# Kernel optimization log

Measured on AMD Instinct MI355X. Metric: run time of the kernel, lower is better.

The kernel has to match this reference:

```python
import jax, jax.numpy as jnp
import numpy as np

N = 131072          # batch of latents
IN_DIM = 64         # in_dim
EMB = 64            # embedding_size
K = 1024            # num_embeddings (codebook size)
DENSE = 2 * (IN_DIM + EMB)  # 256, hidden width of encoder/decoder MLPs


def _linear_params(key, fan_in, fan_out):
    # equinox Linear default init: uniform(-1/sqrt(fan_in), 1/sqrt(fan_in))
    kw, kb = jax.random.split(key)
    lim = 1.0 / np.sqrt(fan_in)
    W = jax.random.uniform(kw, (fan_out, fan_in), minval=-lim, maxval=lim, dtype=jnp.float32)
    b = jax.random.uniform(kb, (fan_out,), minval=-lim, maxval=lim, dtype=jnp.float32)
    return W, b


def setup_inputs() -> dict:
    key = jax.random.key(0)
    ks = jax.random.split(key, 8)
    x = jax.random.normal(ks[0], (N, IN_DIM), dtype=jnp.float32)
    We1, be1 = _linear_params(ks[1], IN_DIM, DENSE)
    We2, be2 = _linear_params(ks[2], DENSE, DENSE)
    We3, be3 = _linear_params(ks[3], DENSE, EMB)
    Wd1, bd1 = _linear_params(ks[4], EMB, DENSE)
    Wd2, bd2 = _linear_params(ks[5], DENSE, DENSE)
    Wd3, bd3 = _linear_params(ks[6], DENSE, IN_DIM)
    emb = jax.random.normal(ks[7], (K, EMB), dtype=jnp.float32) / 1000.0
    return dict(x=x, We1=We1, be1=be1, We2=We2, be2=be2, We3=We3, be3=be3,
                emb=emb, Wd1=Wd1, bd1=bd1, Wd2=Wd2, bd2=bd2, Wd3=Wd3, bd3=bd3)


def reference(x, We1, be1, We2, be2, We3, be3, emb, Wd1, bd1, Wd2, bd2, Wd3, bd3):
    selu = jax.nn.selu
    # encoder: Linear -> selu -> Linear -> selu -> Linear   (batched via matmul)
    h = selu(x @ We1.T + be1)
    h = selu(h @ We2.T + be2)
    z = h @ We3.T + be3                      # [N, EMB]
    # quantize: squared distance to every codebook row, argmin, straight-through
    # ||z - e||^2 expanded to avoid materializing [N, K, EMB]
    d = (jnp.sum(z * z, axis=1, keepdims=True)
         - 2.0 * (z @ emb.T)
         + jnp.sum(emb * emb, axis=1))       # [N, K]
    idx = jnp.argmin(d, axis=1)              # [N] int
    zq = z + jax.lax.stop_gradient(emb[idx] - z)   # straight-through lookup
    # decoder
    h = selu(zq @ Wd1.T + bd1)
    h = selu(h @ Wd2.T + bd2)
    recon = h @ Wd3.T + bd3                  # [N, IN_DIM]
    return recon, idx
```

## Files before the change

### kernel.cpp

```cpp
#include <hip/hip_runtime.h>
#include <math.h>

#pragma clang fp contract(off)

#define NROWS 131072

__device__ __forceinline__ float selu_f(float v) {
    float em  = expm1f(v);
    float neg = 1.6732632423543772f * em;
    float r   = v > 0.0f ? v : neg;
    return 1.0507009873554805f * r;
}

__device__ __forceinline__ float4 ldf4(const float* p) { return *(const float4*)p; }

__device__ __forceinline__ void ld4x4(float4* b, const float* p) {
    b[0] = ldf4(p); b[1] = ldf4(p + 4); b[2] = ldf4(p + 8); b[3] = ldf4(p + 12);
}

__device__ __forceinline__ void fma16a(float* a, const float4* w, float h) {
    a[0]  = __builtin_fmaf(w[0].x, h, a[0]);  a[1]  = __builtin_fmaf(w[0].y, h, a[1]);
    a[2]  = __builtin_fmaf(w[0].z, h, a[2]);  a[3]  = __builtin_fmaf(w[0].w, h, a[3]);
    a[4]  = __builtin_fmaf(w[1].x, h, a[4]);  a[5]  = __builtin_fmaf(w[1].y, h, a[5]);
    a[6]  = __builtin_fmaf(w[1].z, h, a[6]);  a[7]  = __builtin_fmaf(w[1].w, h, a[7]);
    a[8]  = __builtin_fmaf(w[2].x, h, a[8]);  a[9]  = __builtin_fmaf(w[2].y, h, a[9]);
    a[10] = __builtin_fmaf(w[2].z, h, a[10]); a[11] = __builtin_fmaf(w[2].w, h, a[11]);
    a[12] = __builtin_fmaf(w[3].x, h, a[12]); a[13] = __builtin_fmaf(w[3].y, h, a[13]);
    a[14] = __builtin_fmaf(w[3].z, h, a[14]); a[15] = __builtin_fmaf(w[3].w, h, a[15]);
}

__device__ __forceinline__ void step16(float* acc, float4* wb, const float* nextp, float h) {
    float4 t0 = ldf4(nextp), t1 = ldf4(nextp + 4), t2 = ldf4(nextp + 8), t3 = ldf4(nextp + 12);
    fma16a(acc, wb, h);
    wb[0] = t0; wb[1] = t1; wb[2] = t2; wb[3] = t3;
}

__device__ __forceinline__ void fma16q(float* a, float4 w0, float4 w1, float4 w2, float4 w3, float h) {
    a[0]  = __builtin_fmaf(w0.x, h, a[0]);  a[1]  = __builtin_fmaf(w0.y, h, a[1]);
    a[2]  = __builtin_fmaf(w0.z, h, a[2]);  a[3]  = __builtin_fmaf(w0.w, h, a[3]);
    a[4]  = __builtin_fmaf(w1.x, h, a[4]);  a[5]  = __builtin_fmaf(w1.y, h, a[5]);
    a[6]  = __builtin_fmaf(w1.z, h, a[6]);  a[7]  = __builtin_fmaf(w1.w, h, a[7]);
    a[8]  = __builtin_fmaf(w2.x, h, a[8]);  a[9]  = __builtin_fmaf(w2.y, h, a[9]);
    a[10] = __builtin_fmaf(w2.z, h, a[10]); a[11] = __builtin_fmaf(w2.w, h, a[11]);
    a[12] = __builtin_fmaf(w3.x, h, a[12]); a[13] = __builtin_fmaf(w3.y, h, a[13]);
    a[14] = __builtin_fmaf(w3.z, h, a[14]); a[15] = __builtin_fmaf(w3.w, h, a[15]);
}

typedef __attribute__((address_space(3))) unsigned int lds_u32;
typedef const __attribute__((address_space(1))) unsigned int glb_u32;
__device__ __forceinline__ void gll16(const float* g, float* l) {
    __builtin_amdgcn_global_load_lds((glb_u32*)g, (lds_u32*)l, 16, 0, 0);
}

__global__ void prep_transpose(const float* __restrict__ W1, const float* __restrict__ W2,
                               const float* __restrict__ W3,
                               float* __restrict__ W1T, float* __restrict__ W2T,
                               float* __restrict__ W3T) {
    int id = blockIdx.x * 256 + threadIdx.x;
    if (id < 65536) { int c = id >> 8, j = id & 255; W2T[j * 256 + c] = W2[id]; }
    int id2 = id - 65536;
    if (id2 >= 0 && id2 < 16384) { int e = id2 >> 8, c = id2 & 255; W3T[c * 64 + e] = W3[id2]; }
    int id3 = id - 81920;
    if (id3 >= 0 && id3 < 16384) { int c = id3 >> 6, j = id3 & 63; W1T[j * 256 + c] = W1[id3]; }
}

__global__ void prep_decoder(const float* __restrict__ emb,
                             const float* __restrict__ Wd1, const float* __restrict__ bd1,
                             const float* __restrict__ Wd2, const float* __restrict__ bd2,
                             const float* __restrict__ Wd3, const float* __restrict__ bd3,
                             float* __restrict__ dec_out, float* __restrict__ en) {
    __shared__ float e[64];
    __shared__ float h1[256];
    __shared__ float h2[256];
    const int t = threadIdx.x;
    for (int kc = 0; kc < 4; ++kc) {
        const int k = blockIdx.x * 4 + kc;
        __syncthreads();
        if (t < 64) e[t] = emb[k * 64 + t];
        __syncthreads();
        {
            float acc = 0.0f;
            const float* w = Wd1 + t * 64;
            #pragma unroll
            for (int j = 0; j < 64; ++j) acc = __builtin_fmaf(w[j], e[j], acc);
            h1[t] = selu_f(acc + bd1[t]);
        }
        __syncthreads();
        {
            float acc = 0.0f;
            const float* w = Wd2 + t * 256;
            #pragma unroll 8
            for (int j = 0; j < 256; ++j) acc = __builtin_fmaf(w[j], h1[j], acc);
            h2[t] = selu_f(acc + bd2[t]);
        }
        __syncthreads();
        if (t < 64) {
            float acc = 0.0f;
            const float* w = Wd3 + t * 256;
            #pragma unroll 8
            for (int j = 0; j < 256; ++j) acc = __builtin_fmaf(w[j], h2[j], acc);
            dec_out[k * 64 + t] = acc + bd3[t];
        }
        if (t == 0) {
            float r[8];
            #pragma unroll
            for (int u = 0; u < 8; ++u) r[u] = e[u] * e[u];
            #pragma unroll
            for (int i = 8; i < 64; i += 8) {
                #pragma unroll
                for (int u = 0; u < 8; ++u) { float p = e[i + u] * e[i + u]; r[u] = r[u] + p; }
            }
            en[k] = ((r[0] + r[1]) + (r[2] + r[3])) + ((r[4] + r[5]) + (r[6] + r[7]));
        }
    }
}

__global__ __launch_bounds__(256) __attribute__((amdgpu_waves_per_eu(2, 8)))
void vqvae_main(const float* __restrict__ x,
                const float* __restrict__ b1, const float* __restrict__ b2,
                const float* __restrict__ b3,
                const float* __restrict__ W1T, const float* __restrict__ W2T,
                const float* __restrict__ W3T,
                const float* __restrict__ emb, const float* __restrict__ en,
                const float* __restrict__ dec_out, float* __restrict__ out) {
    __shared__ __align__(16) float B0[4096];
    __shared__ __align__(16) float B1[4352];
    __shared__ __align__(16) float B2[4096];

    const int t    = threadIdx.x;
    const int wave = t >> 6;
    const int lane = t & 63;
    const size_t rowbase = (size_t)blockIdx.x * 64;

    int lz;
    asm volatile("v_mov_b32 %0, 0" : "=v"(lz));

    const float* W1Tv = W1T + lz;
    const float* W2Tv = W2T + lz;
    const float* W3Tv = W3T + lz;
    const float* b1v  = b1 + lz;
    const float* b2v  = b2 + lz;
    const float* b3v  = b3 + lz;
    const float* env  = en + lz;
    const float* embv = emb + lz;

    #pragma unroll
    for (int q = 0; q < 4; ++q) {
        int f = t + 256 * q;
        int r = f >> 4, c4 = f & 15;
        float4 v = ldf4(x + (rowbase + r) * 64 + c4 * 4);
        B0[(c4 * 4 + 0) * 64 + r] = v.x;
        B0[(c4 * 4 + 1) * 64 + r] = v.y;
        B0[(c4 * 4 + 2) * 64 + r] = v.z;
        B0[(c4 * 4 + 3) * 64 + r] = v.w;
    }
    __syncthreads();

    float acc2[64];
    #pragma unroll
    for (int u = 0; u < 64; ++u) acc2[u] = 0.0f;

    for (int cc = 0; cc < 4; ++cc) {
        {
            const float* wp = W1Tv + cc * 64 + wave * 16;
            float4 A[4];
            ld4x4(A, wp);
            float acc[16];
            #pragma unroll
            for (int u = 0; u < 16; ++u) acc[u] = 0.0f;
            #pragma unroll 1
            for (int j = 0; j < 64; ++j) {
                const float* np = wp + (j + 1) * 256;
                step16(acc, A, np, B0[j * 64 + lane]);
            }
            float bb[16];
            *(float4*)&bb[0]  = ldf4(b1v + cc * 64 + wave * 16);
            *(float4*)&bb[4]  = ldf4(b1v + cc * 64 + wave * 16 + 4);
            *(float4*)&bb[8]  = ldf4(b1v + cc * 64 + wave * 16 + 8);
            *(float4*)&bb[12] = ldf4(b1v + cc * 64 + wave * 16 + 12);
            float hv[16];
            #pragma unroll
            for (int u = 0; u < 16; ++u) hv[u] = selu_f(acc[u] + bb[u]);
            #pragma unroll
            for (int up = 0; up < 8; ++up) {
                *(float2*)&B1[(wave * 8 + up) * 128 + (lane << 1)] =
                    make_float2(hv[2 * up], hv[2 * up + 1]);
            }
        }
        __syncthreads();
        {
            const float* gsrc = W2Tv + (size_t)(cc * 64 + (lane >> 4)) * 256 + wave * 64 + (lane & 15) * 4;
            float* stA = B2 + wave * 1024;
            gll16(gsrc, stA);
            gll16(gsrc + 1024, stA + 256);
            #pragma unroll 1
            for (int s = 0; s < 8; ++s) {
                if (s < 7) {
                    const float* ns = gsrc + (size_t)(s + 1) * 2048;
                    float* nd = stA + ((s + 1) & 1) * 512;
                    gll16(ns, nd);
                    gll16(ns + 1024, nd + 256);
                    asm volatile("s_waitcnt vmcnt(2)" ::: "memory");
                } else {
                    asm volatile("s_waitcnt vmcnt(0)" ::: "memory");
                }
                const float* wl = stA + (s & 1) * 512;
                #pragma unroll
                for (int jj = 0; jj < 8; jj += 2) {
                    float2 h01 = *(const float2*)&B1[((s * 8 + jj) >> 1) * 128 + (lane << 1)];
                    const float* r0 = wl + jj * 64;
                    #pragma unroll
                    for (int qd = 0; qd < 4; ++qd) {
                        const float* p = r0 + qd * 16;
                        fma16q(acc2 + qd * 16, ldf4(p), ldf4(p + 4), ldf4(p + 8), ldf4(p + 12), h01.x);
                    }
                    const float* r1 = wl + (jj + 1) * 64;
                    #pragma unroll
                    for (int qd = 0; qd < 4; ++qd) {
                        const float* p = r1 + qd * 16;
                        fma16q(acc2 + qd * 16, ldf4(p), ldf4(p + 4), ldf4(p + 8), ldf4(p + 12), h01.y);
                    }
                }
            }
        }
        __syncthreads();
    }

    {
        #pragma unroll
        for (int qd = 0; qd < 4; ++qd) {
            float bb[16];
            *(float4*)&bb[0]  = ldf4(b2v + wave * 64 + qd * 16);
            *(float4*)&bb[4]  = ldf4(b2v + wave * 64 + qd * 16 + 4);
            *(float4*)&bb[8]  = ldf4(b2v + wave * 64 + qd * 16 + 8);
            *(float4*)&bb[12] = ldf4(b2v + wave * 64 + qd * 16 + 12);
            #pragma unroll
            for (int i = 0; i < 16; ++i)
                acc2[qd * 16 + i] = selu_f(acc2[qd * 16 + i] + bb[i]);
        }
    }

    const int er = wave * 16;
    float s01[16], s23[16];
    for (int g = 0; g < 4; ++g) {
        if (wave == g) {
            #pragma unroll
            for (int u = 0; u < 64; ++u) B0[u * 64 + lane] = acc2[u];
        }
        __syncthreads();
        const float* w3p = W3Tv + g * 4096 + er;
        float4 F0[4], F1[4];
        ld4x4(F0, w3p); ld4x4(F1, w3p + 64);
        float P[16];
        #pragma unroll
        for (int u = 0; u < 16; ++u) P[u] = 0.0f;
        #pragma unroll 1
        for (int c = 0; c < 64; c += 2) {
            const float* np = w3p + (c + 2) * 64;
            step16(P, F0, np,      B0[(c + 0) * 64 + lane]);
            step16(P, F1, np + 64, B0[(c + 1) * 64 + lane]);
        }
        if (g == 0) {
            #pragma unroll
            for (int u = 0; u < 16; ++u) s01[u] = P[u];
        } else if (g == 1) {
            #pragma unroll
            for (int u = 0; u < 16; ++u) s01[u] = s01[u] + P[u];
        } else if (g == 2) {
            #pragma unroll
            for (int u = 0; u < 16; ++u) s23[u] = P[u];
        } else {
            #pragma unroll
            for (int u = 0; u < 16; ++u) s23[u] = s23[u] + P[u];
        }
        __syncthreads();
    }

    {
        float bb[16];
        *(float4*)&bb[0]  = ldf4(b3v + er);
        *(float4*)&bb[4]  = ldf4(b3v + er + 4);
        *(float4*)&bb[8]  = ldf4(b3v + er + 8);
        *(float4*)&bb[12] = ldf4(b3v + er + 12);
        float zv[16];
        #pragma unroll
        for (int u = 0; u < 16; ++u) zv[u] = (s01[u] + s23[u]) + bb[u];
        #pragma unroll
        for (int m = 0; m < 4; ++m)
            *(float4*)&B1[lane * 68 + er + m * 4] =
                make_float4(zv[4 * m], zv[4 * m + 1], zv[4 * m + 2], zv[4 * m + 3]);
    }
    __syncthreads();

    const int k0 = wave * 256;
    {
        float4 ev = ldf4(env + k0 + lane * 4);
        *(float4*)&B2[wave * 256 + lane * 4] = ev;
    }
    const float* esrc = embv + (size_t)(k0 + (lane >> 4)) * 64 + (lane & 15) * 4;
    float* eA = B0 + wave * 1024;
    gll16(esrc, eA);
    gll16(esrc + 256, eA + 256);

    float A;
    {
        float r[8];
        {
            float4 v0 = *(const float4*)&B1[lane * 68 + 0];
            float4 v1 = *(const float4*)&B1[lane * 68 + 4];
            r[0] = v0.x * v0.x; r[1] = v0.y * v0.y; r[2] = v0.z * v0.z; r[3] = v0.w * v0.w;
            r[4] = v1.x * v1.x; r[5] = v1.y * v1.y; r[6] = v1.z * v1.z; r[7] = v1.w * v1.w;
        }
        #pragma unroll
        for (int i = 8; i < 64; i += 8) {
            float4 v0 = *(const float4*)&B1[lane * 68 + i];
            float4 v1 = *(const float4*)&B1[lane * 68 + i + 4];
            float p0 = v0.x * v0.x, p1 = v0.y * v0.y, p2 = v0.z * v0.z, p3 = v0.w * v0.w;
            float p4 = v1.x * v1.x, p5 = v1.y * v1.y, p6 = v1.z * v1.z, p7 = v1.w * v1.w;
            r[0] = r[0] + p0; r[1] = r[1] + p1; r[2] = r[2] + p2; r[3] = r[3] + p3;
            r[4] = r[4] + p4; r[5] = r[5] + p5; r[6] = r[6] + p6; r[7] = r[7] + p7;
        }
        A = ((r[0] + r[1]) + (r[2] + r[3])) + ((r[4] + r[5]) + (r[6] + r[7]));
    }

    float best = 3.4e38f;
    int bk = k0;
    #pragma unroll 1
    for (int kc = 0; kc < 256; kc += 8) {
        const int cur = (kc >> 3) & 1;
        if (kc < 248) {
            const float* ns = esrc + (size_t)(kc + 8) * 64;
            float* nd = eA + (cur ^ 1) * 512;
            gll16(ns, nd);
            gll16(ns + 256, nd + 256);
            asm volatile("s_waitcnt vmcnt(2)" ::: "memory");
        } else {
            asm volatile("s_waitcnt vmcnt(0)" ::: "memory");
        }
        const float* ebase = eA + cur * 512;
        float d0[8], d1[8], d2[8], d3[8];
        #pragma unroll
        for (int c = 0; c < 8; ++c) { d0[c] = 0.f; d1[c] = 0.f; d2[c] = 0.f; d3[c] = 0.f; }
        #pragma unroll
        for (int q = 0; q < 4; ++q) {
            float4 zq0 = *(const float4*)&B1[lane * 68 + q * 16];
            float4 zq1 = *(const float4*)&B1[lane * 68 + q * 16 + 4];
            float4 zq2 = *(const float4*)&B1[lane * 68 + q * 16 + 8];
            float4 zq3 = *(const float4*)&B1[lane * 68 + q * 16 + 12];
            #pragma unroll
            for (int c = 0; c < 8; ++c) {
                const float* ep = ebase + c * 64 + q * 16;
                float4 e0 = ldf4(ep), e1 = ldf4(ep + 4), e2 = ldf4(ep + 8), e3 = ldf4(ep + 12);
                d0[c] = __builtin_fmaf(zq0.x, e0.x, d0[c]);
                d1[c] = __builtin_fmaf(zq0.y, e0.y, d1[c]);
                d2[c] = __builtin_fmaf(zq0.z, e0.z, d2[c]);
                d3[c] = __builtin_fmaf(zq0.w, e0.w, d3[c]);
                d0[c] = __builtin_fmaf(zq1.x, e1.x, d0[c]);
                d1[c] = __builtin_fmaf(zq1.y, e1.y, d1[c]);
                d2[c] = __builtin_fmaf(zq1.z, e1.z, d2[c]);
                d3[c] = __builtin_fmaf(zq1.w, e1.w, d3[c]);
                d0[c] = __builtin_fmaf(zq2.x, e2.x, d0[c]);
                d1[c] = __builtin_fmaf(zq2.y, e2.y, d1[c]);
                d2[c] = __builtin_fmaf(zq2.z, e2.z, d2[c]);
                d3[c] = __builtin_fmaf(zq2.w, e2.w, d3[c]);
                d0[c] = __builtin_fmaf(zq3.x, e3.x, d0[c]);
                d1[c] = __builtin_fmaf(zq3.y, e3.y, d1[c]);
                d2[c] = __builtin_fmaf(zq3.z, e3.z, d2[c]);
                d3[c] = __builtin_fmaf(zq3.w, e3.w, d3[c]);
            }
        }
        float enb[8];
        *(float4*)&enb[0] = *(const float4*)&B2[wave * 256 + kc];
        *(float4*)&enb[4] = *(const float4*)&B2[wave * 256 + kc + 4];
        #pragma unroll
        for (int c = 0; c < 8; ++c) {
            float dot = (d0[c] + d1[c]) + (d2[c] + d3[c]);
            float tt  = __builtin_fmaf(-2.0f, dot, A);
            float s   = tt + enb[c];
            if (s < best) { best = s; bk = k0 + kc + c; }
        }
    }
    __syncthreads();

    float* cand_s = B0 + 64;
    int*   cand_k = ((int*)B0) + 320;
    int*   ixp    = (int*)B0;
    cand_s[wave * 64 + lane] = best;
    cand_k[wave * 64 + lane] = bk;
    __syncthreads();
    if (t < 64) {
        float s0 = cand_s[t];
        int   kk = cand_k[t];
        #pragma unroll
        for (int w2 = 1; w2 < 4; ++w2) {
            float sw = cand_s[w2 * 64 + t];
            if (sw < s0) { s0 = sw; kk = cand_k[w2 * 64 + t]; }
        }
        ixp[t] = kk;
        out[(size_t)NROWS * 64 + rowbase + t] = (float)kk;
    }
    __syncthreads();

    #pragma unroll
    for (int q = 0; q < 4; ++q) {
        int f = t + 256 * q;
        int r = f >> 4, c4 = f & 15;
        float4 v = ldf4(dec_out + (size_t)ixp[r] * 64 + c4 * 4);
        *(float4*)(out + (rowbase + r) * 64 + c4 * 4) = v;
    }
}

extern "C" void kernel_launch(void* const* d_in, const int* in_sizes, int n_in,
                              void* d_out, int out_size, void* d_ws, size_t ws_size,
                              hipStream_t stream) {
    const float* x   = (const float*)d_in[0];
    const float* We1 = (const float*)d_in[1];
    const float* be1 = (const float*)d_in[2];
    const float* We2 = (const float*)d_in[3];
    const float* be2 = (const float*)d_in[4];
    const float* We3 = (const float*)d_in[5];
    const float* be3 = (const float*)d_in[6];
    const float* emb = (const float*)d_in[7];
    const float* Wd1 = (const float*)d_in[8];
    const float* bd1 = (const float*)d_in[9];
    const float* Wd2 = (const float*)d_in[10];
    const float* bd2 = (const float*)d_in[11];
    const float* Wd3 = (const float*)d_in[12];
    const float* bd3 = (const float*)d_in[13];
    float* out = (float*)d_out;

    float* ws      = (float*)d_ws;
    float* dec_out = ws;
    float* W2T     = ws + 65536;
    float* W1T     = ws + 131072;
    float* W3T     = ws + 147456;
    float* en      = ws + 163840;

    prep_transpose<<<384, 256, 0, stream>>>(We1, We2, We3, W1T, W2T, W3T);
    prep_decoder<<<256, 256, 0, stream>>>(emb, Wd1, bd1, Wd2, bd2, Wd3, bd3, dec_out, en);
    vqvae_main<<<NROWS / 64, 256, 0, stream>>>(x, be1, be2, be3, W1T, W2T, W3T, emb, en,
                                               dec_out, out);
}
```

Before: 1.270 ms.

## Cut register pressure to raise occupancy to three waves per EU

Raises the minimum waves-per-EU hint from 2 to 3, which forces the compiler into a tighter register budget. To fit that budget it shrinks several live register sets: layer-2 FMAs are grouped in 8-wide chunks, the W3 prefetch double-buffer is dropped, the codebook distance loop handles 4 codes per step with a single async LDS load, and bias pointers no longer go through the zero-offset VGPR trick. The goal is more resident waves to hide memory and LDS latency. The cost is less software prefetching, more loop iterations and waits per code, and possible register spills.

```diff
diff --git a/kernel.cpp b/kernel.cpp
--- a/kernel.cpp
+++ b/kernel.cpp
@@ -14,8 +14,17 @@
 
 __device__ __forceinline__ float4 ldf4(const float* p) { return *(const float4*)p; }
 
+__device__ __forceinline__ void ld2x4(float4* b, const float* p) { b[0] = ldf4(p); b[1] = ldf4(p + 4); }
+
 __device__ __forceinline__ void ld4x4(float4* b, const float* p) {
     b[0] = ldf4(p); b[1] = ldf4(p + 4); b[2] = ldf4(p + 8); b[3] = ldf4(p + 12);
+}
+
+__device__ __forceinline__ void fma8a(float* a, const float4* w, float h) {
+    a[0] = __builtin_fmaf(w[0].x, h, a[0]);  a[1] = __builtin_fmaf(w[0].y, h, a[1]);
+    a[2] = __builtin_fmaf(w[0].z, h, a[2]);  a[3] = __builtin_fmaf(w[0].w, h, a[3]);
+    a[4] = __builtin_fmaf(w[1].x, h, a[4]);  a[5] = __builtin_fmaf(w[1].y, h, a[5]);
+    a[6] = __builtin_fmaf(w[1].z, h, a[6]);  a[7] = __builtin_fmaf(w[1].w, h, a[7]);
 }
 
 __device__ __forceinline__ void fma16a(float* a, const float4* w, float h) {
@@ -33,17 +42,6 @@
     float4 t0 = ldf4(nextp), t1 = ldf4(nextp + 4), t2 = ldf4(nextp + 8), t3 = ldf4(nextp + 12);
     fma16a(acc, wb, h);
     wb[0] = t0; wb[1] = t1; wb[2] = t2; wb[3] = t3;
-}
-
-__device__ __forceinline__ void fma16q(float* a, float4 w0, float4 w1, float4 w2, float4 w3, float h) {
-    a[0]  = __builtin_fmaf(w0.x, h, a[0]);  a[1]  = __builtin_fmaf(w0.y, h, a[1]);
-    a[2]  = __builtin_fmaf(w0.z, h, a[2]);  a[3]  = __builtin_fmaf(w0.w, h, a[3]);
-    a[4]  = __builtin_fmaf(w1.x, h, a[4]);  a[5]  = __builtin_fmaf(w1.y, h, a[5]);
-    a[6]  = __builtin_fmaf(w1.z, h, a[6]);  a[7]  = __builtin_fmaf(w1.w, h, a[7]);
-    a[8]  = __builtin_fmaf(w2.x, h, a[8]);  a[9]  = __builtin_fmaf(w2.y, h, a[9]);
-    a[10] = __builtin_fmaf(w2.z, h, a[10]); a[11] = __builtin_fmaf(w2.w, h, a[11]);
-    a[12] = __builtin_fmaf(w3.x, h, a[12]); a[13] = __builtin_fmaf(w3.y, h, a[13]);
-    a[14] = __builtin_fmaf(w3.z, h, a[14]); a[15] = __builtin_fmaf(w3.w, h, a[15]);
 }
 
 typedef __attribute__((address_space(3))) unsigned int lds_u32;
@@ -115,7 +113,7 @@
     }
 }
 
-__global__ __launch_bounds__(256) __attribute__((amdgpu_waves_per_eu(2, 8)))
+__global__ __launch_bounds__(256) __attribute__((amdgpu_waves_per_eu(3, 8)))
 void vqvae_main(const float* __restrict__ x,
                 const float* __restrict__ b1, const float* __restrict__ b2,
                 const float* __restrict__ b3,
@@ -138,9 +136,6 @@
     const float* W1Tv = W1T + lz;
     const float* W2Tv = W2T + lz;
     const float* W3Tv = W3T + lz;
-    const float* b1v  = b1 + lz;
-    const float* b2v  = b2 + lz;
-    const float* b3v  = b3 + lz;
     const float* env  = en + lz;
     const float* embv = emb + lz;
 
@@ -174,10 +169,10 @@
                 step16(acc, A, np, B0[j * 64 + lane]);
             }
             float bb[16];
-            *(float4*)&bb[0]  = ldf4(b1v + cc * 64 + wave * 16);
-            *(float4*)&bb[4]  = ldf4(b1v + cc * 64 + wave * 16 + 4);
-            *(float4*)&bb[8]  = ldf4(b1v + cc * 64 + wave * 16 + 8);
-            *(float4*)&bb[12] = ldf4(b1v + cc * 64 + wave * 16 + 12);
+            *(float4*)&bb[0]  = ldf4(b1 + cc * 64 + wave * 16);
+            *(float4*)&bb[4]  = ldf4(b1 + cc * 64 + wave * 16 + 4);
+            *(float4*)&bb[8]  = ldf4(b1 + cc * 64 + wave * 16 + 8);
+            *(float4*)&bb[12] = ldf4(b1 + cc * 64 + wave * 16 + 12);
             float hv[16];
             #pragma unroll
             for (int u = 0; u < 16; ++u) hv[u] = selu_f(acc[u] + bb[u]);
@@ -210,15 +205,17 @@
                     float2 h01 = *(const float2*)&B1[((s * 8 + jj) >> 1) * 128 + (lane << 1)];
                     const float* r0 = wl + jj * 64;
                     #pragma unroll
-                    for (int qd = 0; qd < 4; ++qd) {
-                        const float* p = r0 + qd * 16;
-                        fma16q(acc2 + qd * 16, ldf4(p), ldf4(p + 4), ldf4(p + 8), ldf4(p + 12), h01.x);
+                    for (int g8 = 0; g8 < 8; ++g8) {
+                        float4 wv[2];
+                        ld2x4(wv, r0 + g8 * 8);
+                        fma8a(acc2 + g8 * 8, wv, h01.x);
                     }
                     const float* r1 = wl + (jj + 1) * 64;
                     #pragma unroll
-                    for (int qd = 0; qd < 4; ++qd) {
-                        const float* p = r1 + qd * 16;
-                        fma16q(acc2 + qd * 16, ldf4(p), ldf4(p + 4), ldf4(p + 8), ldf4(p + 12), h01.y);
+                    for (int g8 = 0; g8 < 8; ++g8) {
+                        float4 wv[2];
+                        ld2x4(wv, r1 + g8 * 8);
+                        fma8a(acc2 + g8 * 8, wv, h01.y);
                     }
                 }
             }
@@ -230,10 +227,10 @@
         #pragma unroll
         for (int qd = 0; qd < 4; ++qd) {
             float bb[16];
-            *(float4*)&bb[0]  = ldf4(b2v + wave * 64 + qd * 16);
-            *(float4*)&bb[4]  = ldf4(b2v + wave * 64 + qd * 16 + 4);
-            *(float4*)&bb[8]  = ldf4(b2v + wave * 64 + qd * 16 + 8);
-            *(float4*)&bb[12] = ldf4(b2v + wave * 64 + qd * 16 + 12);
+            *(float4*)&bb[0]  = ldf4(b2 + wave * 64 + qd * 16);
+            *(float4*)&bb[4]  = ldf4(b2 + wave * 64 + qd * 16 + 4);
+            *(float4*)&bb[8]  = ldf4(b2 + wave * 64 + qd * 16 + 8);
+            *(float4*)&bb[12] = ldf4(b2 + wave * 64 + qd * 16 + 12);
             #pragma unroll
             for (int i = 0; i < 16; ++i)
                 acc2[qd * 16 + i] = selu_f(acc2[qd * 16 + i] + bb[i]);
@@ -249,16 +246,14 @@
         }
         __syncthreads();
         const float* w3p = W3Tv + g * 4096 + er;
-        float4 F0[4], F1[4];
-        ld4x4(F0, w3p); ld4x4(F1, w3p + 64);
         float P[16];
         #pragma unroll
         for (int u = 0; u < 16; ++u) P[u] = 0.0f;
         #pragma unroll 1
-        for (int c = 0; c < 64; c += 2) {
-            const float* np = w3p + (c + 2) * 64;
-            step16(P, F0, np,      B0[(c + 0) * 64 + lane]);
-            step16(P, F1, np + 64, B0[(c + 1) * 64 + lane]);
+        for (int c = 0; c < 64; ++c) {
+            float4 F[4];
+            ld4x4(F, w3p + c * 64);
+            fma16a(P, F, B0[c * 64 + lane]);
         }
         if (g == 0) {
             #pragma unroll
@@ -278,10 +273,10 @@
 
     {
         float bb[16];
-        *(float4*)&bb[0]  = ldf4(b3v + er);
-        *(float4*)&bb[4]  = ldf4(b3v + er + 4);
-        *(float4*)&bb[8]  = ldf4(b3v + er + 8);
-        *(float4*)&bb[12] = ldf4(b3v + er + 12);
+        *(float4*)&bb[0]  = ldf4(b3 + er);
+        *(float4*)&bb[4]  = ldf4(b3 + er + 4);
+        *(float4*)&bb[8]  = ldf4(b3 + er + 8);
+        *(float4*)&bb[12] = ldf4(b3 + er + 12);
         float zv[16];
         #pragma unroll
         for (int u = 0; u < 16; ++u) zv[u] = (s01[u] + s23[u]) + bb[u];
@@ -300,7 +295,6 @@
     const float* esrc = embv + (size_t)(k0 + (lane >> 4)) * 64 + (lane & 15) * 4;
     float* eA = B0 + wave * 1024;
     gll16(esrc, eA);
-    gll16(esrc + 256, eA + 256);
 
     float A;
     {
@@ -326,21 +320,18 @@
     float best = 3.4e38f;
     int bk = k0;
     #pragma unroll 1
-    for (int kc = 0; kc < 256; kc += 8) {
-        const int cur = (kc >> 3) & 1;
-        if (kc < 248) {
-            const float* ns = esrc + (size_t)(kc + 8) * 64;
-            float* nd = eA + (cur ^ 1) * 512;
-            gll16(ns, nd);
-            gll16(ns + 256, nd + 256);
-            asm volatile("s_waitcnt vmcnt(2)" ::: "memory");
+    for (int kc = 0; kc < 256; kc += 4) {
+        const int cur = (kc >> 2) & 1;
+        if (kc < 252) {
+            gll16(esrc + (size_t)(kc + 4) * 64, eA + (cur ^ 1) * 256);
+            asm volatile("s_waitcnt vmcnt(1)" ::: "memory");
         } else {
             asm volatile("s_waitcnt vmcnt(0)" ::: "memory");
         }
-        const float* ebase = eA + cur * 512;
-        float d0[8], d1[8], d2[8], d3[8];
-        #pragma unroll
-        for (int c = 0; c < 8; ++c) { d0[c] = 0.f; d1[c] = 0.f; d2[c] = 0.f; d3[c] = 0.f; }
+        const float* ebase = eA + cur * 256;
+        float d0[4], d1[4], d2[4], d3[4];
+        #pragma unroll
+        for (int c = 0; c < 4; ++c) { d0[c] = 0.f; d1[c] = 0.f; d2[c] = 0.f; d3[c] = 0.f; }
         #pragma unroll
         for (int q = 0; q < 4; ++q) {
             float4 zq0 = *(const float4*)&B1[lane * 68 + q * 16];
@@ -348,7 +339,7 @@
             float4 zq2 = *(const float4*)&B1[lane * 68 + q * 16 + 8];
             float4 zq3 = *(const float4*)&B1[lane * 68 + q * 16 + 12];
             #pragma unroll
-            for (int c = 0; c < 8; ++c) {
+            for (int c = 0; c < 4; ++c) {
                 const float* ep = ebase + c * 64 + q * 16;
                 float4 e0 = ldf4(ep), e1 = ldf4(ep + 4), e2 = ldf4(ep + 8), e3 = ldf4(ep + 12);
                 d0[c] = __builtin_fmaf(zq0.x, e0.x, d0[c]);
@@ -369,11 +360,10 @@
                 d3[c] = __builtin_fmaf(zq3.w, e3.w, d3[c]);
             }
         }
-        float enb[8];
+        float enb[4];
         *(float4*)&enb[0] = *(const float4*)&B2[wave * 256 + kc];
-        *(float4*)&enb[4] = *(const float4*)&B2[wave * 256 + kc + 4];
-        #pragma unroll
-        for (int c = 0; c < 8; ++c) {
+        #pragma unroll
+        for (int c = 0; c < 4; ++c) {
             float dot = (d0[c] + d1[c]) + (d2[c] + d3[c]);
             float tt  = __builtin_fmaf(-2.0f, dot, A);
             float s   = tt + enb[c];
```

After: 1.142 ms. 10.1% less time.
